# Performance work log

Hardware: AMD Instinct MI355X
Metric: run time of the kernel (lower is better)

## Reference

```python
import jax, jax.numpy as jnp
import numpy as np

B, IDIM, ODIM, MSIZE = 8192, 4096, 4096, 128
ICOUNT = (IDIM + MSIZE - 1) // MSIZE        # 32
MCOUNT = (max(IDIM, ODIM) + MSIZE - 1) // MSIZE  # 32
OCOUNT = (ODIM + MSIZE - 1) // MSIZE        # 32


def setup_inputs() -> dict:
    key = jax.random.key(0)
    ks = jax.random.split(key, 7)
    s_in = 1.0 / np.sqrt(ICOUNT)
    s_m = 1.0 / np.sqrt(MSIZE)
    s_out = 1.0 / np.sqrt(MCOUNT)
    return {
        "x": jax.random.normal(ks[0], (B, IDIM), dtype=jnp.float32),
        "W_in": jax.random.normal(ks[1], (MCOUNT, ICOUNT), dtype=jnp.float32) * s_in,
        "b_in": jax.random.normal(ks[2], (MCOUNT,), dtype=jnp.float32) * s_in,
        "W_mods": jax.random.normal(ks[3], (MCOUNT, MSIZE, MSIZE), dtype=jnp.float32) * s_m,
        "b_mods": jax.random.normal(ks[4], (MCOUNT, MSIZE), dtype=jnp.float32) * s_m,
        "W_out": jax.random.normal(ks[5], (OCOUNT, MCOUNT), dtype=jnp.float32) * s_out,
        "b_out": jax.random.normal(ks[6], (OCOUNT,), dtype=jnp.float32) * s_out,
        "odim": ODIM,
    }


def reference(x, W_in, b_in, W_mods, b_mods, W_out, b_out, odim):
    msize = W_mods.shape[-1]
    b = x.shape[0]
    idim = x.shape[-1]
    rem = idim % msize  # static
    if rem != 0:
        x = jnp.pad(x, ((0, 0), (0, msize - rem)))
    icount = x.shape[-1] // msize
    # reshape to blocks then tail_permute (swap last two axes)
    x = x.reshape(b, icount, msize).swapaxes(-1, -2)      # [B, msize, icount]
    x = jnp.einsum('bmi,ci->bmc', x, W_in) + b_in          # fcin -> [B, msize, mcount]
    x = x.swapaxes(-1, -2)                                 # [B, mcount, msize]
    # per-block submodule: Linear(msize->msize) per block, vectorized over blocks
    x = jnp.einsum('bcm,cnm->bcn', x, W_mods) + b_mods     # [B, mcount, msize]
    x = x.swapaxes(-1, -2)                                 # [B, msize, mcount]
    x = jnp.einsum('bmc,oc->bmo', x, W_out) + b_out        # fcout -> [B, msize, ocount]
    x = x.reshape(b, -1)[:, :odim]                         # [B, odim]
    return x  # act = Identity
```

## Files before the change

kernel.cpp:

```cpp
#include <hip/hip_runtime.h>
#include <stdint.h>


#define BT    16
#define NTHR  1024
#define GRID  512
#define IDIM  4096
#define ODIM  4096

typedef __attribute__((ext_vector_type(8))) __bf16 bf16x8;
typedef __attribute__((ext_vector_type(4))) float  floatx4;

union BF8 { uint32_t w[4]; unsigned short h[8]; bf16x8 v; };

__device__ __forceinline__ unsigned short f2bf(float f) {
    uint32_t u = __builtin_bit_cast(uint32_t, f);
    u += 0x7fffu + ((u >> 16) & 1u);
    return (unsigned short)(u >> 16);
}

#define XP_BT 40
#define XP_M  656
#define YP_BT 40
#define YP_C  648
#define WP_BT 34
#define WP_N  546
#define WBUF  8736

template<bool WBF16>
__global__ __launch_bounds__(NTHR, 4)
void tinymod_fused(const float* __restrict__ x,
                   const float* __restrict__ W_in,
                   const float* __restrict__ b_in,
                   const void*  __restrict__ wmods,
                   const float* __restrict__ b_mods,
                   const float* __restrict__ W_out,
                   const float* __restrict__ b_out,
                   float* __restrict__ out)
{
    __shared__ unsigned short xs[32 * XP_M] __attribute__((aligned(16)));
    __shared__ unsigned short ys[32 * YP_C] __attribute__((aligned(16)));
    __shared__ unsigned short wc[2 * WBUF]  __attribute__((aligned(16)));

    const int tid  = threadIdx.x;
    const int w    = tid >> 6;
    const int lane = tid & 63;
    const int l15  = lane & 15;
    const int grp  = lane >> 4;
    const int row0 = blockIdx.x * BT;

    const int cc = w >> 3, mq = w & 7;

    BF8 winf;
    {
        const float* p = W_in + (l15 + 16*cc) * 32 + grp * 8;
        #pragma unroll
        for (int j = 0; j < 8; j++) winf.h[j] = f2bf(p[j]);
    }
    const float bin = b_in[l15 + 16*cc];

    const int smp = tid & 31, sbt = (tid >> 5) & 15, sih = tid >> 9;
    const float* xb = x + (row0 + sbt) * IDIM + smp + sih * (16 * 128);

    floatx4 acc[2][8];
    #pragma unroll
    for (int a = 0; a < 2; a++)
        #pragma unroll
        for (int b = 0; b < 8; b++) acc[a][b] = (floatx4){0.f, 0.f, 0.f, 0.f};

    const unsigned short* __restrict__ wm16 = (const unsigned short*)wmods;
    const float*          __restrict__ wm32 = (const float*)wmods;
    int wmb[2];
    #pragma unroll
    for (int c2 = 0; c2 < 2; c2++)
        wmb[c2] = ((2*w + c2) * 128 + l15) * 128 + grp * 8;

    float xr[16];
    #pragma unroll
    for (int j = 0; j < 16; j++) xr[j] = xb[j * 128];

    #pragma unroll
    for (int mc = 0; mc < 4; mc++) {
        #pragma unroll
        for (int p = 0; p < 2; p++) {
            BF8 t;
            #pragma unroll
            for (int j = 0; j < 8; j++) t.h[j] = f2bf(xr[p*8 + j]);
            uint4 v4; v4.x = t.w[0]; v4.y = t.w[1]; v4.z = t.w[2]; v4.w = t.w[3];
            *(uint4*)&xs[smp*XP_M + sbt*XP_BT + sih*16 + p*8] = v4;
        }
        __syncthreads();

        unsigned short yh[4][4];
        #pragma unroll
        for (int k = 0; k < 4; k++) {
            BF8 a;
            const uint4 av = *(const uint4*)&xs[(mq*4 + k)*XP_M + l15*XP_BT + grp*8];
            a.w[0] = av.x; a.w[1] = av.y; a.w[2] = av.z; a.w[3] = av.w;
            floatx4 y = {0.f, 0.f, 0.f, 0.f};
            y = __builtin_amdgcn_mfma_f32_16x16x32_bf16(a.v, winf.v, y, 0, 0, 0);
            #pragma unroll
            for (int r = 0; r < 4; r++) yh[k][r] = f2bf(y[r] + bin);
        }
        #pragma unroll
        for (int r = 0; r < 4; r++) {
            uint2 pk;
            pk.x = (uint32_t)yh[0][r] | ((uint32_t)yh[1][r] << 16);
            pk.y = (uint32_t)yh[2][r] | ((uint32_t)yh[3][r] << 16);
            *(uint2*)&ys[(l15 + 16*cc)*YP_C + (grp*4 + r)*YP_BT + mq*4] = pk;
        }
        __syncthreads();

        float xr2[16];
        if (mc < 3) {
            #pragma unroll
            for (int j = 0; j < 16; j++) xr2[j] = xb[j*128 + (mc + 1)*32];
        }

        #pragma unroll
        for (int c2 = 0; c2 < 2; c2++) {
            BF8 a;
            const uint4 av = *(const uint4*)&ys[(2*w + c2)*YP_C + l15*YP_BT + grp*8];
            a.w[0] = av.x; a.w[1] = av.y; a.w[2] = av.z; a.w[3] = av.w;
            #pragma unroll
            for (int nt = 0; nt < 8; nt++) {
                BF8 b;
                if (WBF16) {
                    const uint4 bv = *(const uint4*)&wm16[wmb[c2] + nt*2048 + mc*32];
                    b.w[0] = bv.x; b.w[1] = bv.y; b.w[2] = bv.z; b.w[3] = bv.w;
                } else {
                    const float* wp = wm32 + wmb[c2] + nt*2048 + mc*32;
                    #pragma unroll
                    for (int j = 0; j < 8; j++) b.h[j] = f2bf(wp[j]);
                }
                acc[c2][nt] = __builtin_amdgcn_mfma_f32_16x16x32_bf16(a.v, b.v, acc[c2][nt], 0, 0, 0);
            }
        }
        if (mc < 3) {
            #pragma unroll
            for (int j = 0; j < 16; j++) xr[j] = xr2[j];
        }
    }

    BF8 woutf[2];
    #pragma unroll
    for (int oc = 0; oc < 2; oc++) {
        const float* q = W_out + (l15 + 16*oc) * 32 + grp * 8;
        #pragma unroll
        for (int j = 0; j < 8; j++) woutf[oc].h[j] = f2bf(q[j]);
    }
    const float bo0 = b_out[l15], bo1 = b_out[16 + l15];
    float bm[2][8];
    #pragma unroll
    for (int c2 = 0; c2 < 2; c2++)
        #pragma unroll
        for (int nt = 0; nt < 8; nt++)
            bm[c2][nt] = b_mods[(2*w + c2)*128 + nt*16 + l15];

    float* outb = out + (long)row0 * ODIM;
    #pragma unroll
    for (int nt = 0; nt < 8; nt++) {
        const int buf = (nt & 1) * WBUF;
        #pragma unroll
        for (int r = 0; r < 4; r++) {
            const uint32_t pk = (uint32_t)f2bf(acc[0][nt][r] + bm[0][nt])
                              | ((uint32_t)f2bf(acc[1][nt][r] + bm[1][nt]) << 16);
            *(uint32_t*)&wc[buf + l15*WP_N + (grp*4 + r)*WP_BT + 2*w] = pk;
        }
        __syncthreads();
        BF8 a;
        #pragma unroll
        for (int j = 0; j < 4; j++)
            a.w[j] = *(const uint32_t*)&wc[buf + w*WP_N + l15*WP_BT + grp*8 + j*2];
        #pragma unroll
        for (int oc = 0; oc < 2; oc++) {
            floatx4 v = {0.f, 0.f, 0.f, 0.f};
            v = __builtin_amdgcn_mfma_f32_16x16x32_bf16(a.v, woutf[oc].v, v, 0, 0, 0);
            const float bo = oc ? bo1 : bo0;
            float* po = outb + (nt*16 + w)*32 + oc*16 + l15;
            #pragma unroll
            for (int r = 0; r < 4; r++)
                po[(grp*4 + r) * ODIM] = v[r] + bo;
        }
    }
}

__global__ void wmods_to_bf16(const float* __restrict__ wsrc, unsigned short* __restrict__ o) {
    const int i = (blockIdx.x * 256 + threadIdx.x) * 4;
    const float4 f = *(const float4*)(wsrc + i);
    uint2 pk;
    pk.x = (uint32_t)f2bf(f.x) | ((uint32_t)f2bf(f.y) << 16);
    pk.y = (uint32_t)f2bf(f.z) | ((uint32_t)f2bf(f.w) << 16);
    *(uint2*)(o + i) = pk;
}

extern "C" void kernel_launch(void* const* d_in, const int* in_sizes, int n_in,
                              void* d_out, int out_size, void* d_ws, size_t ws_size,
                              hipStream_t stream)
{
    const float* x     = (const float*)d_in[0];
    const float* W_in  = (const float*)d_in[1];
    const float* b_in  = (const float*)d_in[2];
    const float* Wm    = (const float*)d_in[3];
    const float* b_m   = (const float*)d_in[4];
    const float* W_out = (const float*)d_in[5];
    const float* b_out = (const float*)d_in[6];
    float* out = (float*)d_out;

    const size_t wm_elems = 32u * 128u * 128u;
    if (ws_size >= wm_elems * sizeof(unsigned short)) {
        unsigned short* wbf = (unsigned short*)d_ws;
        wmods_to_bf16<<<(int)(wm_elems / (256 * 4)), 256, 0, stream>>>(Wm, wbf);
        tinymod_fused<true><<<GRID, NTHR, 0, stream>>>(x, W_in, b_in, (const void*)wbf,
                                                       b_m, W_out, b_out, out);
    } else {
        tinymod_fused<false><<<GRID, NTHR, 0, stream>>>(x, W_in, b_in, (const void*)Wm,
                                                        b_m, W_out, b_out, out);
    }
}
```

Baseline: 342.5 us.

## Split fused kernel into fcin and mods+fcout kernels with bf16 intermediate

When the workspace is large enough, the single fused kernel is replaced by two kernels. The first computes fcin and writes a bf16 intermediate of shape [B,32,128] (64 MB) to global memory. The second runs the per-block Linear plus fcout, reading that intermediate and the bf16 W_mods directly from global memory. The aim is to cut shared-memory use and barriers per block so more blocks fit per CU, at the cost of an extra 128 MB of global round-trip traffic and one more launch.

```diff
diff --git a/kernel.cpp b/kernel.cpp
--- a/kernel.cpp
+++ b/kernel.cpp
@@ -2,9 +2,6 @@
 #include <stdint.h>
 
 
-#define BT    16
-#define NTHR  1024
-#define GRID  512
 #define IDIM  4096
 #define ODIM  4096
 
@@ -19,6 +16,175 @@
     return (unsigned short)(u >> 16);
 }
 
+#define XP1_BT 40
+#define XP1_M  656
+#define XS1    (16 * XP1_M)
+
+__global__ __launch_bounds__(512, 6)
+void k1_fcin(const float* __restrict__ x,
+             const float* __restrict__ W_in,
+             const float* __restrict__ b_in,
+             unsigned short* __restrict__ y)
+{
+    __shared__ unsigned short xs[2 * XS1] __attribute__((aligned(16)));
+
+    const int tid  = threadIdx.x;
+    const int w    = tid >> 6;
+    const int lane = tid & 63;
+    const int l15  = lane & 15;
+    const int grp  = lane >> 4;
+    const int row0 = blockIdx.x * 16;
+
+    const int mq = w & 3, cc = w >> 2;
+    BF8 winf;
+    {
+        const float* p = W_in + (l15 + 16*cc) * 32 + grp * 8;
+        #pragma unroll
+        for (int j = 0; j < 8; j++) winf.h[j] = f2bf(p[j]);
+    }
+    const float bin = b_in[l15 + 16*cc];
+
+    const int smp = tid & 15, sbt = (tid >> 4) & 15, sih = tid >> 8;
+    const float* xb = x + (row0 + sbt) * IDIM + sih * (16 * 128) + smp;
+
+    float xr[16];
+    #pragma unroll
+    for (int j = 0; j < 16; j++) xr[j] = xb[j * 128];
+
+    for (int mc = 0; mc < 8; mc++) {
+        unsigned short* buf = &xs[(mc & 1) * XS1];
+        #pragma unroll
+        for (int p = 0; p < 2; p++) {
+            BF8 t;
+            #pragma unroll
+            for (int j = 0; j < 8; j++) t.h[j] = f2bf(xr[p*8 + j]);
+            uint4 v4; v4.x = t.w[0]; v4.y = t.w[1]; v4.z = t.w[2]; v4.w = t.w[3];
+            *(uint4*)&buf[smp*XP1_M + sbt*XP1_BT + sih*16 + p*8] = v4;
+        }
+        __syncthreads();
+
+        if (mc < 7) {
+            #pragma unroll
+            for (int j = 0; j < 16; j++) xr[j] = xb[j*128 + (mc + 1)*16];
+        }
+
+        unsigned short yh[4][4];
+        #pragma unroll
+        for (int k = 0; k < 4; k++) {
+            BF8 a;
+            const uint4 av = *(const uint4*)&buf[(mq*4 + k)*XP1_M + l15*XP1_BT + grp*8];
+            a.w[0] = av.x; a.w[1] = av.y; a.w[2] = av.z; a.w[3] = av.w;
+            floatx4 yv = {0.f, 0.f, 0.f, 0.f};
+            yv = __builtin_amdgcn_mfma_f32_16x16x32_bf16(a.v, winf.v, yv, 0, 0, 0);
+            #pragma unroll
+            for (int r = 0; r < 4; r++) yh[k][r] = f2bf(yv[r] + bin);
+        }
+        #pragma unroll
+        for (int r = 0; r < 4; r++) {
+            uint2 pk;
+            pk.x = (uint32_t)yh[0][r] | ((uint32_t)yh[1][r] << 16);
+            pk.y = (uint32_t)yh[2][r] | ((uint32_t)yh[3][r] << 16);
+            *(uint2*)&y[((row0 + grp*4 + r) * 32 + (l15 + 16*cc)) * 128 + mc*16 + mq*4] = pk;
+        }
+    }
+}
+
+#define WP2_BT 36
+#define WP2_N  580
+#define WC2    (32 * WP2_N)
+
+__global__ __launch_bounds__(512, 4)
+void k2_mods_out(const unsigned short* __restrict__ y,
+                 const unsigned short* __restrict__ wm16,
+                 const float* __restrict__ b_mods,
+                 const float* __restrict__ W_out,
+                 const float* __restrict__ b_out,
+                 float* __restrict__ out)
+{
+    __shared__ unsigned short wc[WC2] __attribute__((aligned(16)));
+
+    const int tid  = threadIdx.x;
+    const int w    = tid >> 6;
+    const int lane = tid & 63;
+    const int l15  = lane & 15;
+    const int grp  = lane >> 4;
+    const int row0 = blockIdx.x * 16;
+
+    BF8 woutf[2];
+    #pragma unroll
+    for (int oc = 0; oc < 2; oc++) {
+        const float* q = W_out + (l15 + 16*oc) * 32 + grp * 8;
+        #pragma unroll
+        for (int j = 0; j < 8; j++) woutf[oc].h[j] = f2bf(q[j]);
+    }
+    const float bo0 = b_out[l15], bo1 = b_out[16 + l15];
+
+    for (int ntq = 0; ntq < 4; ntq++) {
+        floatx4 acc[4][2];
+        #pragma unroll
+        for (int ci = 0; ci < 4; ci++)
+            #pragma unroll
+            for (int nh = 0; nh < 2; nh++) acc[ci][nh] = (floatx4){0.f,0.f,0.f,0.f};
+
+        #pragma unroll
+        for (int ci = 0; ci < 4; ci++) {
+            const int c = w*4 + ci;
+            const unsigned short* yc = y + ((long)(row0 + l15) * 32 + c) * 128 + grp*8;
+            const unsigned short* wb = wm16 + ((long)(c*128 + ntq*32 + l15)) * 128 + grp*8;
+            #pragma unroll
+            for (int kc = 0; kc < 4; kc++) {
+                BF8 a;
+                const uint4 av = *(const uint4*)&yc[kc*32];
+                a.w[0] = av.x; a.w[1] = av.y; a.w[2] = av.z; a.w[3] = av.w;
+                #pragma unroll
+                for (int nh = 0; nh < 2; nh++) {
+                    BF8 b;
+                    const uint4 bv = *(const uint4*)&wb[nh*16*128 + kc*32];
+                    b.w[0] = bv.x; b.w[1] = bv.y; b.w[2] = bv.z; b.w[3] = bv.w;
+                    acc[ci][nh] = __builtin_amdgcn_mfma_f32_16x16x32_bf16(a.v, b.v, acc[ci][nh], 0, 0, 0);
+                }
+            }
+        }
+        #pragma unroll
+        for (int nh = 0; nh < 2; nh++) {
+            const float bm0 = b_mods[(w*4 + 0)*128 + ntq*32 + nh*16 + l15];
+            const float bm1 = b_mods[(w*4 + 1)*128 + ntq*32 + nh*16 + l15];
+            const float bm2 = b_mods[(w*4 + 2)*128 + ntq*32 + nh*16 + l15];
+            const float bm3 = b_mods[(w*4 + 3)*128 + ntq*32 + nh*16 + l15];
+            #pragma unroll
+            for (int r = 0; r < 4; r++) {
+                uint2 pk;
+                pk.x = (uint32_t)f2bf(acc[0][nh][r] + bm0) | ((uint32_t)f2bf(acc[1][nh][r] + bm1) << 16);
+                pk.y = (uint32_t)f2bf(acc[2][nh][r] + bm2) | ((uint32_t)f2bf(acc[3][nh][r] + bm3) << 16);
+                *(uint2*)&wc[(nh*16 + l15)*WP2_N + (grp*4 + r)*WP2_BT + w*4] = pk;
+            }
+        }
+        __syncthreads();
+
+        #pragma unroll
+        for (int k = 0; k < 4; k++) {
+            const int nloc = w*4 + k;
+            BF8 a;
+            const uint4 av = *(const uint4*)&wc[nloc*WP2_N + l15*WP2_BT + grp*8];
+            a.w[0] = av.x; a.w[1] = av.y; a.w[2] = av.z; a.w[3] = av.w;
+            #pragma unroll
+            for (int oc = 0; oc < 2; oc++) {
+                floatx4 v = {0.f, 0.f, 0.f, 0.f};
+                v = __builtin_amdgcn_mfma_f32_16x16x32_bf16(a.v, woutf[oc].v, v, 0, 0, 0);
+                const float bo = oc ? bo1 : bo0;
+                float* po = out + (long)(row0) * ODIM + (ntq*32 + nloc)*32 + oc*16 + l15;
+                #pragma unroll
+                for (int r = 0; r < 4; r++)
+                    po[(long)(grp*4 + r) * ODIM] = v[r] + bo;
+            }
+        }
+        __syncthreads();
+    }
+}
+
+#define BT    16
+#define NTHR  1024
+#define GRID  512
 #define XP_BT 40
 #define XP_M  656
 #define YP_BT 40
@@ -48,7 +214,6 @@
     const int l15  = lane & 15;
     const int grp  = lane >> 4;
     const int row0 = blockIdx.x * BT;
-
     const int cc = w >> 3, mq = w & 7;
 
     BF8 winf;
@@ -97,10 +262,10 @@
             BF8 a;
             const uint4 av = *(const uint4*)&xs[(mq*4 + k)*XP_M + l15*XP_BT + grp*8];
             a.w[0] = av.x; a.w[1] = av.y; a.w[2] = av.z; a.w[3] = av.w;
-            floatx4 y = {0.f, 0.f, 0.f, 0.f};
-            y = __builtin_amdgcn_mfma_f32_16x16x32_bf16(a.v, winf.v, y, 0, 0, 0);
-            #pragma unroll
-            for (int r = 0; r < 4; r++) yh[k][r] = f2bf(y[r] + bin);
+            floatx4 yv = {0.f, 0.f, 0.f, 0.f};
+            yv = __builtin_amdgcn_mfma_f32_16x16x32_bf16(a.v, winf.v, yv, 0, 0, 0);
+            #pragma unroll
+            for (int r = 0; r < 4; r++) yh[k][r] = f2bf(yv[r] + bin);
         }
         #pragma unroll
         for (int r = 0; r < 4; r++) {
@@ -207,10 +372,18 @@
     const float* b_out = (const float*)d_in[6];
     float* out = (float*)d_out;
 
-    const size_t wm_elems = 32u * 128u * 128u;
-    if (ws_size >= wm_elems * sizeof(unsigned short)) {
+    const size_t wm_bytes = 32u * 128u * 128u * sizeof(unsigned short);
+    const size_t y_bytes  = (size_t)8192 * 32 * 128 * sizeof(unsigned short);
+
+    if (ws_size >= wm_bytes + y_bytes) {
         unsigned short* wbf = (unsigned short*)d_ws;
-        wmods_to_bf16<<<(int)(wm_elems / (256 * 4)), 256, 0, stream>>>(Wm, wbf);
+        unsigned short* y   = (unsigned short*)((char*)d_ws + wm_bytes);
+        wmods_to_bf16<<<512, 256, 0, stream>>>(Wm, wbf);
+        k1_fcin<<<512, 512, 0, stream>>>(x, W_in, b_in, y);
+        k2_mods_out<<<512, 512, 0, stream>>>(y, wbf, b_m, W_out, b_out, out);
+    } else if (ws_size >= wm_bytes) {
+        unsigned short* wbf = (unsigned short*)d_ws;
+        wmods_to_bf16<<<512, 256, 0, stream>>>(Wm, wbf);
         tinymod_fused<true><<<GRID, NTHR, 0, stream>>>(x, W_in, b_in, (const void*)wbf,
                                                        b_m, W_out, b_out, out);
     } else {
```

Measured after the change: 369.3 us. +7.8%, slower.
